# Kernel optimization log

Hardware: AMD Instinct MI355X
Metric: run time of the kernel (lower is better)

## Reference

```python
import jax, jax.numpy as jnp
import numpy as np

B, CIN, COUT = 4, 256, 256
H, W = 48, 48
KH = KW = 7
SH = SW = 1
PH = PW = 3
REL = COUT // 2  # rel_size with groups=1


def setup_inputs() -> dict:
    key = jax.random.key(0)
    ks = jax.random.split(key, 7)
    fan = float(CIN)
    x = jax.random.normal(ks[0], (B, CIN, H, W), jnp.float32)
    w_q = jax.random.normal(ks[1], (COUT, CIN), jnp.float32) * (2.0 / fan) ** 0.5
    w_k = jax.random.normal(ks[2], (COUT, CIN), jnp.float32) * (2.0 / fan) ** 0.5
    w_v = jax.random.normal(ks[3], (COUT, CIN), jnp.float32) * (2.0 / fan) ** 0.5
    bound = 1.0 / np.sqrt(COUT)
    bias = jax.random.uniform(ks[4], (1, COUT, 1, 1), jnp.float32, -bound, bound)
    rel_x = jax.random.normal(ks[5], (REL, KW), jnp.float32)
    rel_y = jax.random.normal(ks[6], (COUT - REL, KH), jnp.float32)
    return {"x": x, "w_q": w_q, "w_k": w_k, "w_v": w_v, "bias": bias,
            "rel_x": rel_x, "rel_y": rel_y}


def reference(x, w_q, w_k, w_v, bias, rel_x, rel_y):
    b = x.shape[0]
    ph, pw = H + 2 * PH, W + 2 * PW
    fh = (ph - KH) // SH + 1
    fw = (pw - KW) // SW + 1
    xp = jnp.pad(x, ((0, 0), (0, 0), (PH, PH), (PW, PW)))
    # 1x1 convs (groups=1) as channel matmuls
    vq = jnp.einsum('oc,bchw->bohw', w_q, xp)
    vk = jnp.einsum('oc,bchw->bohw', w_k, xp)
    vv = jnp.einsum('oc,bchw->bohw', w_v, xp)
    # query at window centers: [b, C, fh, fw]
    win_q = vq[:, :, (KH - 1) // 2: ph - KH // 2: SH, (KW - 1) // 2: pw - KW // 2: SW]
    # relative position terms (sum over channel halves)
    qx = jnp.einsum('bxhw,xk->bhwk', win_q[:, :REL], rel_x)        # [b,fh,fw,kw]
    qy = jnp.einsum('byhw,yk->bhwk', win_q[:, REL:], rel_y)        # [b,fh,fw,kh]
    # overlapping windows via gather (equivalent to torch unfold)
    I = jnp.arange(fh)[:, None] * SH + jnp.arange(KH)[None, :]     # [fh,kh]
    J = jnp.arange(fw)[:, None] * SW + jnp.arange(KW)[None, :]     # [fw,kw]
    win_k = vk[:, :, I[:, None, :, None], J[None, :, None, :]]     # [b,C,fh,fw,kh,kw]
    # channel-summed attention logits (shared across channels, as in source)
    scores = jnp.einsum('bchw,bchwkl->bhwkl', win_q, win_k)
    scores = scores + qy[:, :, :, :, None] + qx[:, :, :, None, :]
    attn = jax.nn.softmax(scores.reshape(b, fh, fw, KH * KW), axis=-1)
    attn = attn.reshape(b, fh, fw, KH, KW)
    win_v = vv[:, :, I[:, None, :, None], J[None, :, None, :]]     # [b,C,fh,fw,kh,kw]
    out = jnp.einsum('bhwkl,bchwkl->bchw', attn, win_v) + bias
    return out
```

## Files before the change

kernel.cpp:

```cpp
#include <hip/hip_runtime.h>

#define BB 4
#define CC 256
#define HH 48
#define WW 48
#define HWHW 2304
#define KK 49
#define RELN 128

#define QSZ (BB*CC*HWHW)
#define ATTNOFF (3*QSZ)
#define SBUF_FLOATS (BB*HH*64*WW)
#define WTOFF (ATTNOFF + SBUF_FLOATS)
#define WT_FLOATS 196608
#define KBOFF (WTOFF + WT_FLOATS)
#define KB_FLOATS 3145728
#define RBOFF (KBOFF + KB_FLOATS)

typedef short bf16x8 __attribute__((ext_vector_type(8)));
typedef float f32x4 __attribute__((ext_vector_type(4)));

__device__ __forceinline__ void split_bf16(float f, unsigned short& hi, unsigned short& lo)
{
    unsigned u = __float_as_uint(f);
    hi = (unsigned short)(u >> 16);
    float r = f - __uint_as_float(u & 0xFFFF0000u);
    unsigned v = __float_as_uint(r);
    v += 0x7FFFu + ((v >> 16) & 1u);
    lo = (unsigned short)(v >> 16);
}

__device__ __forceinline__ void gload16(const uint4* g, uint4* l)
{
    __builtin_amdgcn_global_load_lds(
        (const __attribute__((address_space(1))) void*)g,
        (__attribute__((address_space(3))) void*)l, 16, 0, 0);
}

__global__ __launch_bounds__(256) void prep_kernel(
    const float* __restrict__ x,
    const float* __restrict__ wq, const float* __restrict__ wk,
    const float* __restrict__ wvp,
    const float* __restrict__ relx, const float* __restrict__ rely,
    unsigned short* __restrict__ xt, unsigned short* __restrict__ wt,
    float* __restrict__ ws)
{
    __shared__ unsigned short lds[32*520];
    const int bid = blockIdx.x;
    const int t = threadIdx.x;

    if (bid < 288) {
        const int b = bid / 72;
        const int hw0 = (bid % 72) * 32;
        const int hw = t & 31, cp = t >> 5;
        #pragma unroll 4
        for (int i = 0; i < 32; ++i) {
            int c = i*8 + cp;
            float f = x[((size_t)b*CC + c)*HWHW + hw0 + hw];
            unsigned short hi, lo; split_bf16(f, hi, lo);
            int ch = i*2;
            lds[hw*520 + ((ch       ^ (hw&7))*8) + cp] = hi;
            lds[hw*520 + (((ch + 1) ^ (hw&7))*8) + cp] = lo;
        }
        __syncthreads();
        const int hw2 = t >> 3, u = t & 7;
        uint4* xt4 = (uint4*)xt;
        const size_t rowbase = ((size_t)b*HWHW + hw0 + hw2) * 64;
        #pragma unroll
        for (int j = 0; j < 8; ++j) {
            int chunk = j*8 + u;
            uint4 v = *(const uint4*)&lds[hw2*520 + chunk*8];
            xt4[rowbase + chunk] = v;
        }
        return;
    }
    if (bid < 384) {
        const int tt = (bid - 288)*256 + t;
        const int m = tt >> 5, kg = tt & 31;
        const float* src = (m < 256) ? wq : (m < 512) ? wk : wvp;
        const float* row = src + (size_t)(m & 255)*256 + kg*8;
        unsigned short h[8], l[8];
        #pragma unroll
        for (int j = 0; j < 8; ++j) split_bf16(row[j], h[j], l[j]);
        uint4 hv, lv;
        hv.x = (unsigned)h[0] | ((unsigned)h[1]<<16); hv.y = (unsigned)h[2] | ((unsigned)h[3]<<16);
        hv.z = (unsigned)h[4] | ((unsigned)h[5]<<16); hv.w = (unsigned)h[6] | ((unsigned)h[7]<<16);
        lv.x = (unsigned)l[0] | ((unsigned)l[1]<<16); lv.y = (unsigned)l[2] | ((unsigned)l[3]<<16);
        lv.z = (unsigned)l[4] | ((unsigned)l[5]<<16); lv.w = (unsigned)l[6] | ((unsigned)l[7]<<16);
        uint4* dstrow = (uint4*)wt + (size_t)m*64;
        const int ks = kg >> 2, s_hi = 2*(kg & 3);
        dstrow[ks*8 + ( s_hi      ^ (m&7))] = hv;
        dstrow[ks*8 + ((s_hi + 1) ^ (m&7))] = lv;
        return;
    }
    if (bid < 1152) {
        f32x4* kbz = (f32x4*)(ws + KBOFF);
        int i0 = (bid - 384)*256 + t;
        f32x4 z = (f32x4){0.f,0.f,0.f,0.f};
        #pragma unroll
        for (int it = 0; it < 4; ++it) kbz[i0 + it*196608] = z;
        return;
    }
    {
        unsigned short* rb = (unsigned short*)(ws + RBOFF);
        #pragma unroll
        for (int it = 0; it < 4; ++it) {
            int idx = t + it*256;
            int gi  = idx & 7;
            int l   = (idx >> 3) & 15;
            int ck4 = (idx >> 7) & 3;
            int rel = idx >> 9;
            int isLo = gi >> 2, g4i = gi & 3;
            unsigned short vals[8];
            #pragma unroll
            for (int j = 0; j < 8; ++j) {
                int cl = ck4*32 + g4i*8 + j;
                float f = (l < 7) ? (rel ? rely[cl*7 + l] : relx[cl*7 + l]) : 0.f;
                unsigned short hi, lo; split_bf16(f, hi, lo);
                vals[j] = isLo ? lo : hi;
            }
            int slot = gi ^ (l & 7);
            unsigned short* dst = rb + (((size_t)rel*4 + ck4)*16 + l)*64 + slot*8;
            uint4 pack;
            pack.x = (unsigned)vals[0] | ((unsigned)vals[1]<<16);
            pack.y = (unsigned)vals[2] | ((unsigned)vals[3]<<16);
            pack.z = (unsigned)vals[4] | ((unsigned)vals[5]<<16);
            pack.w = (unsigned)vals[6] | ((unsigned)vals[7]<<16);
            *(uint4*)dst = pack;
        }
    }
}

__global__ __launch_bounds__(256) void proj_gemm_kernel(
    const unsigned short* __restrict__ xt,
    const unsigned short* __restrict__ wt,
    float* __restrict__ ws)
{
    __shared__ uint4 smem[2][1024];
    const int n0 = blockIdx.x * 64;
    const int m0 = blockIdx.y * 64;
    const int b = n0 / HWHW;
    const int hwb = n0 % HWHW;
    const int tid = threadIdx.x;
    const int wid = tid >> 6, ln = tid & 63;
    const int wm = wid >> 1, wn = wid & 1;
    const int l15 = ln & 15, g = ln >> 4;

    f32x4 acc[2][2];
    #pragma unroll
    for (int i = 0; i < 2; ++i)
        #pragma unroll
        for (int j = 0; j < 2; ++j) acc[i][j] = (f32x4){0.f,0.f,0.f,0.f};

    const uint4* wt4 = (const uint4*)wt;
    const uint4* xt4 = (const uint4*)xt;
    const int lrow = ln >> 3, lslot = ln & 7;

    #define STAGE(bf, ks)                                                          \
        {                                                                          \
            _Pragma("unroll")                                                      \
            for (int i = 0; i < 2; ++i) {                                          \
                int seg = wid*2 + i;                                               \
                int row = seg*8 + lrow;                                            \
                gload16(wt4 + (size_t)(m0 + row)*64 + (ks)*8 + lslot,              \
                        &smem[bf][seg*64]);                                        \
                gload16(xt4 + (size_t)(n0 + row)*64 + (ks)*8 + lslot,              \
                        &smem[bf][512 + seg*64]);                                  \
            }                                                                      \
        }

    STAGE(0, 0);
    #pragma unroll
    for (int ks = 0; ks < 8; ++ks) {
        const int cur = ks & 1;
        if (ks < 7) STAGE(cur ^ 1, ks + 1);
        if (ks < 7) asm volatile("s_waitcnt vmcnt(4)" ::: "memory");
        else        asm volatile("s_waitcnt vmcnt(0)" ::: "memory");
        __builtin_amdgcn_s_barrier();
        __builtin_amdgcn_sched_barrier(0);
        bf16x8 aH[2], aL[2], bH[2], bL[2];
        #pragma unroll
        for (int mt = 0; mt < 2; ++mt) {
            int rA = wm*32 + mt*16 + l15;
            aH[mt] = *(const bf16x8*)&smem[cur][rA*8 + ((2*g)   ^ (rA&7))];
            aL[mt] = *(const bf16x8*)&smem[cur][rA*8 + ((2*g+1) ^ (rA&7))];
        }
        #pragma unroll
        for (int nt = 0; nt < 2; ++nt) {
            int rB = wn*32 + nt*16 + l15;
            bH[nt] = *(const bf16x8*)&smem[cur][512 + rB*8 + ((2*g)   ^ (rB&7))];
            bL[nt] = *(const bf16x8*)&smem[cur][512 + rB*8 + ((2*g+1) ^ (rB&7))];
        }
        #pragma unroll
        for (int mt = 0; mt < 2; ++mt)
            #pragma unroll
            for (int nt = 0; nt < 2; ++nt) {
                acc[mt][nt] = __builtin_amdgcn_mfma_f32_16x16x32_bf16(aH[mt], bH[nt], acc[mt][nt], 0, 0, 0);
                acc[mt][nt] = __builtin_amdgcn_mfma_f32_16x16x32_bf16(aH[mt], bL[nt], acc[mt][nt], 0, 0, 0);
                acc[mt][nt] = __builtin_amdgcn_mfma_f32_16x16x32_bf16(aL[mt], bH[nt], acc[mt][nt], 0, 0, 0);
            }
        if (ks < 7) {
            asm volatile("s_waitcnt lgkmcnt(0)" ::: "memory");
            __builtin_amdgcn_s_barrier();
        }
    }
    #undef STAGE

    const int proj = m0 >> 8;
    #pragma unroll
    for (int mt = 0; mt < 2; ++mt) {
        int chb = (m0 & 255) + wm*32 + mt*16 + 4*g;
        #pragma unroll
        for (int nt = 0; nt < 2; ++nt) {
            int hw = hwb + wn*32 + nt*16 + l15;
            f32x4 v = acc[mt][nt];
            if (proj == 2) {
                int ch4 = chb >> 2;
                float* dst = ws + (size_t)2*QSZ + (((size_t)b*64 + ch4)*HWHW + hw)*4;
                *(f32x4*)dst = v;
            } else {
                int hh = hw / 48, w = hw % 48;
                int ck = chb >> 5, p = chb & 31;
                unsigned short h0,h1,h2,h3,l0,l1,l2,l3;
                split_bf16(v[0],h0,l0); split_bf16(v[1],h1,l1);
                split_bf16(v[2],h2,l2); split_bf16(v[3],h3,l3);
                uint2 hv, lv;
                hv.x = (unsigned)h0 | ((unsigned)h1<<16); hv.y = (unsigned)h2 | ((unsigned)h3<<16);
                lv.x = (unsigned)l0 | ((unsigned)l1<<16); lv.y = (unsigned)l2 | ((unsigned)l3<<16);
                int g8 = p >> 3, half = (p >> 2) & 1;
                unsigned short* tb; size_t rowbase; int key;
                if (proj == 0) {
                    tb = (unsigned short*)ws;
                    rowbase = ((((size_t)b*8 + ck)*48 + hh)*48 + w)*64;
                    key = w & 7;
                } else {
                    tb = (unsigned short*)(ws + KBOFF);
                    rowbase = ((((size_t)b*8 + ck)*48 + hh)*64 + (w+3))*64;
                    key = (w+3) & 7;
                }
                *(uint2*)(tb + rowbase + ((g8 ^ key)*8 + half*4))     = hv;
                *(uint2*)(tb + rowbase + (((g8+4) ^ key)*8 + half*4)) = lv;
            }
        }
    }
}

__global__ __launch_bounds__(512) void scores2_kernel(float* __restrict__ ws)
{
    __shared__ unsigned short sAll[4096*8];
    __shared__ float sc[63][48];

    unsigned short* sQ = sAll;
    unsigned short* sK = sAll + 384*8;
    unsigned short* sR = sAll + 3968*8;

    const int bid = blockIdx.x;
    const int b = bid / 48, h = bid % 48;
    const int tid = threadIdx.x;
    const int wv = tid >> 6, ln = tid & 63;
    const int l15 = ln & 15, g4 = ln >> 4;
    const int key = l15 & 7;

    const unsigned short* QB = (const unsigned short*)ws;
    const unsigned short* KB = (const unsigned short*)(ws + KBOFF);
    const unsigned short* RB = (const unsigned short*)(ws + RBOFF);

    for (int u = tid; u < 63*48; u += 512) ((float*)sc)[u] = 0.f;

    const int dk = wv;
    const int hp = h + dk - 3;
    const bool dok = (wv < 7) && (hp >= 0) && (hp < 48);

    f32x4 acc[6], qx[3], qy[3];
    #pragma unroll
    for (int i = 0; i < 6; ++i) acc[i] = (f32x4){0.f,0.f,0.f,0.f};
    #pragma unroll
    for (int i = 0; i < 3; ++i) { qx[i] = (f32x4){0.f,0.f,0.f,0.f}; qy[i] = (f32x4){0.f,0.f,0.f,0.f}; }

    for (int ck = 0; ck < 8; ++ck) {
        #pragma unroll
        for (int e = 0; e < 8; ++e) {
            const int I = wv*8 + e;
            uint4* dst = (uint4*)sAll + I*64;
            if (I < 6) {
                int unit = I*64 + ln; int row = unit >> 3, gr = unit & 7;
                const uint4* src = (const uint4*)QB
                    + ((((size_t)b*8 + ck)*48 + h)*48 + row)*8 + gr;
                gload16(src, dst);
            } else if (I < 62) {
                int uk = (I-6)*64 + ln;
                int kri = uk >> 9;
                int wi = uk & 511; int row = wi >> 3, gr = wi & 7;
                int kh = h + kri - 3;
                if (kh >= 0 && kh < 48) {
                    const uint4* src = (const uint4*)KB
                        + ((((size_t)b*8 + ck)*48 + kh)*64 + row)*8 + gr;
                    gload16(src, dst);
                }
            } else {
                int ur = (I-62)*64 + ln; int row = ur >> 3, gr = ur & 7;
                int rel = ck >> 2, c4 = ck & 3;
                const uint4* src = (const uint4*)RB
                    + (((size_t)rel*4 + c4)*16 + row)*8 + gr;
                gload16(src, dst);
            }
        }
        __syncthreads();

        bf16x8 AH[3], AL[3];
        #pragma unroll
        for (int i = 0; i < 3; ++i) {
            const unsigned short* qr = sQ + (16*i + l15)*64;
            AH[i] = *(const bf16x8*)(qr + ((g4       ^ key)*8));
            AL[i] = *(const bf16x8*)(qr + (((g4 + 4) ^ key)*8));
        }

        if (wv < 7) {
            if (dok) {
                const unsigned short* kbase = sK + dk*4096;
                bf16x8 BH[4], BL[4];
                #pragma unroll
                for (int j = 0; j < 4; ++j) {
                    const unsigned short* kr = kbase + (j*16 + l15)*64;
                    BH[j] = *(const bf16x8*)(kr + ((g4       ^ key)*8));
                    BL[j] = *(const bf16x8*)(kr + (((g4 + 4) ^ key)*8));
                }
                #pragma unroll
                for (int i = 0; i < 3; ++i) {
                    acc[i*2]   = __builtin_amdgcn_mfma_f32_16x16x32_bf16(AH[i], BH[i],   acc[i*2],   0,0,0);
                    acc[i*2]   = __builtin_amdgcn_mfma_f32_16x16x32_bf16(AH[i], BL[i],   acc[i*2],   0,0,0);
                    acc[i*2]   = __builtin_amdgcn_mfma_f32_16x16x32_bf16(AL[i], BH[i],   acc[i*2],   0,0,0);
                    acc[i*2+1] = __builtin_amdgcn_mfma_f32_16x16x32_bf16(AH[i], BH[i+1], acc[i*2+1], 0,0,0);
                    acc[i*2+1] = __builtin_amdgcn_mfma_f32_16x16x32_bf16(AH[i], BL[i+1], acc[i*2+1], 0,0,0);
                    acc[i*2+1] = __builtin_amdgcn_mfma_f32_16x16x32_bf16(AL[i], BH[i+1], acc[i*2+1], 0,0,0);
                }
            }
        } else {
            const unsigned short* rr = sR + l15*64;
            bf16x8 RH = *(const bf16x8*)(rr + ((g4       ^ key)*8));
            bf16x8 RL = *(const bf16x8*)(rr + (((g4 + 4) ^ key)*8));
            if (ck < 4) {
                #pragma unroll
                for (int i = 0; i < 3; ++i) {
                    qx[i] = __builtin_amdgcn_mfma_f32_16x16x32_bf16(AH[i], RH, qx[i], 0,0,0);
                    qx[i] = __builtin_amdgcn_mfma_f32_16x16x32_bf16(AH[i], RL, qx[i], 0,0,0);
                    qx[i] = __builtin_amdgcn_mfma_f32_16x16x32_bf16(AL[i], RH, qx[i], 0,0,0);
                }
            } else {
                #pragma unroll
                for (int i = 0; i < 3; ++i) {
                    qy[i] = __builtin_amdgcn_mfma_f32_16x16x32_bf16(AH[i], RH, qy[i], 0,0,0);
                    qy[i] = __builtin_amdgcn_mfma_f32_16x16x32_bf16(AH[i], RL, qy[i], 0,0,0);
                    qy[i] = __builtin_amdgcn_mfma_f32_16x16x32_bf16(AL[i], RH, qy[i], 0,0,0);
                }
            }
        }
        __syncthreads();
    }

    const int n = l15;
    if (wv < 7) {
        if (dok) {
            #pragma unroll
            for (int i = 0; i < 3; ++i)
                #pragma unroll
                for (int a = 0; a < 2; ++a) {
                    f32x4 A = acc[i*2+a];
                    #pragma unroll
                    for (int r = 0; r < 4; ++r) {
                        int m = 4*g4 + r;
                        int dl = n - m + a*16;
                        if (dl >= 0 && dl < 7)
                            sc[dk*7 + dl][16*i + m] = A[r];
                    }
                }
        }
    } else {
        if (n < 7) {
            #pragma unroll
            for (int i = 0; i < 3; ++i)
                #pragma unroll
                for (int r = 0; r < 4; ++r) {
                    sc[49 + n][16*i + 4*g4 + r] = qx[i][r];
                    sc[56 + n][16*i + 4*g4 + r] = qy[i][r];
                }
        }
    }
    __syncthreads();

    if (tid < 48) {
        const int w = tid;
        float tot[KK], rx[7], ry[7];
        #pragma unroll
        for (int i = 0; i < KK; ++i) tot[i] = sc[i][w];
        #pragma unroll
        for (int l = 0; l < 7; ++l) { rx[l] = sc[49+l][w]; ry[l] = sc[56+l][w]; }
        float mx = -1e30f;
        #pragma unroll
        for (int dk2 = 0; dk2 < 7; ++dk2)
            #pragma unroll
            for (int dl = 0; dl < 7; ++dl) {
                tot[dk2*7+dl] += ry[dk2] + rx[dl];
                mx = fmaxf(mx, tot[dk2*7+dl]);
            }
        float sum = 0.f;
        #pragma unroll
        for (int i = 0; i < KK; ++i) { float e = __expf(tot[i]-mx); tot[i]=e; sum += e; }
        float inv = 1.f/sum;
        float* base = ws + ATTNOFF + ((size_t)(b*HH + h)*64)*WW + w;
        #pragma unroll
        for (int i = 0; i < KK; ++i) base[(size_t)i*WW] = tot[i]*inv;
    }
}

__global__ __launch_bounds__(128) void pv_kernel(
    const float* __restrict__ bias,
    const float* __restrict__ ws,
    float* __restrict__ out)
{
    const float* vbuf = ws + (size_t)2*QSZ;
    const float* attn = ws + ATTNOFF;

    const int bid = blockIdx.x;
    const int pxt = bid % 18;
    const int pgq = (bid / 18) % 16;
    const int b   = bid / (18*16);

    const int tid = threadIdx.x;
    const int pxg = tid & 31;
    const int pg  = pgq*4 + (tid >> 5);

    const int hw0 = pxt*128 + pxg*4;
    const int w0 = hw0 % WW;
    const int h0 = hw0 / WW;

    const float* vb = vbuf + ((size_t)b*64 + pg)*HWHW*4;
    const float* ab = attn + ((size_t)(b*HH + h0)*64)*WW;

    const float4 b4 = *(const float4*)(bias + pg*4);
    f32x4 bias4 = (f32x4){b4.x, b4.y, b4.z, b4.w};
    f32x4 acc[4];
    #pragma unroll
    for (int p = 0; p < 4; ++p) acc[p] = bias4;

    #pragma unroll
    for (int dk = 0; dk < 7; ++dk) {
        const int gr = h0 + dk - 3;
        const bool rok = (gr >= 0 && gr < HH);
        f32x4 vrow[10];
        #pragma unroll
        for (int jj = 0; jj < 10; ++jj) {
            const int gc = w0 - 3 + jj;
            vrow[jj] = (rok && gc >= 0 && gc < WW)
                ? *(const f32x4*)(vb + ((size_t)gr*WW + gc)*4)
                : (f32x4){0.f,0.f,0.f,0.f};
        }
        const float* arow = ab + (size_t)(dk*7)*WW + w0;
        #pragma unroll
        for (int dl = 0; dl < 7; ++dl) {
            const float4 av = *(const float4*)(arow + (size_t)dl*WW);
            acc[0] += vrow[dl+0] * av.x;
            acc[1] += vrow[dl+1] * av.y;
            acc[2] += vrow[dl+2] * av.z;
            acc[3] += vrow[dl+3] * av.w;
        }
    }
    #pragma unroll
    for (int c = 0; c < 4; ++c) {
        float4 o;
        o.x = acc[0][c]; o.y = acc[1][c]; o.z = acc[2][c]; o.w = acc[3][c];
        *(float4*)(out + ((size_t)b*CC + pg*4 + c)*HWHW + hw0) = o;
    }
}

extern "C" void kernel_launch(void* const* d_in, const int* in_sizes, int n_in,
                              void* d_out, int out_size, void* d_ws, size_t ws_size,
                              hipStream_t stream) {
    const float* x    = (const float*)d_in[0];
    const float* wq   = (const float*)d_in[1];
    const float* wk   = (const float*)d_in[2];
    const float* wv   = (const float*)d_in[3];
    const float* bias = (const float*)d_in[4];
    const float* relx = (const float*)d_in[5];
    const float* rely = (const float*)d_in[6];
    float* ws  = (float*)d_ws;
    float* out = (float*)d_out;
    unsigned short* xt = (unsigned short*)d_out;
    unsigned short* wt = (unsigned short*)(ws + WTOFF);

    prep_kernel<<<dim3(1153), dim3(256), 0, stream>>>(x, wq, wk, wv, relx, rely, xt, wt, ws);
    proj_gemm_kernel<<<dim3(144, 12), dim3(256), 0, stream>>>(xt, wt, ws);
    scores2_kernel<<<dim3(BB*HH), dim3(512), 0, stream>>>(ws);
    pv_kernel<<<dim3(BB*16*18), dim3(128), 0, stream>>>(bias, ws, out);
}
```

Before: 75.15 us.

## Stage Q/K epilogue through LDS for coalesced stores; zero only K padding

```diff
diff --git a/kernel.cpp b/kernel.cpp
--- a/kernel.cpp
+++ b/kernel.cpp
@@ -93,12 +93,18 @@
         dstrow[ks*8 + ((s_hi + 1) ^ (m&7))] = lv;
         return;
     }
-    if (bid < 1152) {
-        f32x4* kbz = (f32x4*)(ws + KBOFF);
-        int i0 = (bid - 384)*256 + t;
-        f32x4 z = (f32x4){0.f,0.f,0.f,0.f};
-        #pragma unroll
-        for (int it = 0; it < 4; ++it) kbz[i0 + it*196608] = z;
+    if (bid < 576) {
+        uint4* kb4 = (uint4*)(ws + KBOFF);
+        const uint4 z = make_uint4(0u,0u,0u,0u);
+        int u0 = (bid - 384)*256 + t;
+        #pragma unroll
+        for (int it = 0; it < 4; ++it) {
+            int u = u0 + it*49152;
+            int bch = u >> 7, rem = u & 127;
+            int r16 = rem >> 3, gr = rem & 7;
+            int r = (r16 < 3) ? r16 : 48 + r16;
+            kb4[((size_t)bch*64 + r)*8 + gr] = z;
+        }
         return;
     }
     {
@@ -207,40 +213,67 @@
     #undef STAGE
 
     const int proj = m0 >> 8;
+    if (proj == 2) {
+        #pragma unroll
+        for (int mt = 0; mt < 2; ++mt) {
+            int chb = (m0 & 255) + wm*32 + mt*16 + 4*g;
+            int ch4 = chb >> 2;
+            #pragma unroll
+            for (int nt = 0; nt < 2; ++nt) {
+                int hw = hwb + wn*32 + nt*16 + l15;
+                float* dst = ws + (size_t)2*QSZ + (((size_t)b*64 + ch4)*HWHW + hw)*4;
+                *(f32x4*)dst = acc[mt][nt];
+            }
+        }
+        return;
+    }
+    __syncthreads();
+    unsigned short* eb = (unsigned short*)&smem[0][0];
     #pragma unroll
     for (int mt = 0; mt < 2; ++mt) {
-        int chb = (m0 & 255) + wm*32 + mt*16 + 4*g;
+        const int chb = (m0 & 255) + wm*32 + mt*16 + 4*g;
+        const int ckl = (chb >> 5) & 1;
+        const int p = chb & 31, g8 = p >> 3, half = (p >> 2) & 1;
         #pragma unroll
         for (int nt = 0; nt < 2; ++nt) {
-            int hw = hwb + wn*32 + nt*16 + l15;
+            const int hwl = wn*32 + nt*16 + l15;
+            const int w = (hwb + hwl) % 48;
+            const int key = (proj == 0 ? w : w + 3) & 7;
             f32x4 v = acc[mt][nt];
-            if (proj == 2) {
-                int ch4 = chb >> 2;
-                float* dst = ws + (size_t)2*QSZ + (((size_t)b*64 + ch4)*HWHW + hw)*4;
-                *(f32x4*)dst = v;
-            } else {
-                int hh = hw / 48, w = hw % 48;
-                int ck = chb >> 5, p = chb & 31;
-                unsigned short h0,h1,h2,h3,l0,l1,l2,l3;
-                split_bf16(v[0],h0,l0); split_bf16(v[1],h1,l1);
-                split_bf16(v[2],h2,l2); split_bf16(v[3],h3,l3);
-                uint2 hv, lv;
-                hv.x = (unsigned)h0 | ((unsigned)h1<<16); hv.y = (unsigned)h2 | ((unsigned)h3<<16);
-                lv.x = (unsigned)l0 | ((unsigned)l1<<16); lv.y = (unsigned)l2 | ((unsigned)l3<<16);
-                int g8 = p >> 3, half = (p >> 2) & 1;
-                unsigned short* tb; size_t rowbase; int key;
-                if (proj == 0) {
-                    tb = (unsigned short*)ws;
-                    rowbase = ((((size_t)b*8 + ck)*48 + hh)*48 + w)*64;
-                    key = w & 7;
-                } else {
-                    tb = (unsigned short*)(ws + KBOFF);
-                    rowbase = ((((size_t)b*8 + ck)*48 + hh)*64 + (w+3))*64;
-                    key = (w+3) & 7;
-                }
-                *(uint2*)(tb + rowbase + ((g8 ^ key)*8 + half*4))     = hv;
-                *(uint2*)(tb + rowbase + (((g8+4) ^ key)*8 + half*4)) = lv;
-            }
+            unsigned short h0,h1,h2,h3,q0,q1,q2,q3;
+            split_bf16(v[0],h0,q0); split_bf16(v[1],h1,q1);
+            split_bf16(v[2],h2,q2); split_bf16(v[3],h3,q3);
+            uint2 hv, lv;
+            hv.x = (unsigned)h0 | ((unsigned)h1<<16); hv.y = (unsigned)h2 | ((unsigned)h3<<16);
+            lv.x = (unsigned)q0 | ((unsigned)q1<<16); lv.y = (unsigned)q2 | ((unsigned)q3<<16);
+            const int base = (ckl*64 + hwl)*64;
+            *(uint2*)(eb + base + ((g8 ^ key)*8 + half*4))     = hv;
+            *(uint2*)(eb + base + (((g8+4) ^ key)*8 + half*4)) = lv;
+        }
+    }
+    __syncthreads();
+    const int ck0 = (m0 & 255) >> 5;
+    if (proj == 0) {
+        const uint4* src = (const uint4*)eb;
+        uint4* qb4 = (uint4*)ws;
+        #pragma unroll
+        for (int ckl2 = 0; ckl2 < 2; ++ckl2) {
+            uint4* dst = qb4 + (((size_t)b*8 + ck0 + ckl2)*HWHW + hwb)*8;
+            #pragma unroll
+            for (int it = 0; it < 2; ++it)
+                dst[tid + it*256] = src[ckl2*512 + tid + it*256];
+        }
+    } else {
+        uint4* kb4 = (uint4*)(ws + KBOFF);
+        const uint4* src = (const uint4*)eb;
+        #pragma unroll
+        for (int it = 0; it < 4; ++it) {
+            int u = tid + it*256;
+            int row = u >> 3, gr = u & 7;
+            int ckl2 = row >> 6, hwl2 = row & 63;
+            int hw2 = hwb + hwl2, h2 = hw2/48, w2 = hw2%48;
+            uint4* dst = kb4 + ((((size_t)b*8 + ck0 + ckl2)*48 + h2)*64 + (w2+3))*8;
+            dst[gr] = src[u];
         }
     }
 }
@@ -488,7 +521,7 @@
     unsigned short* xt = (unsigned short*)d_out;
     unsigned short* wt = (unsigned short*)(ws + WTOFF);
 
-    prep_kernel<<<dim3(1153), dim3(256), 0, stream>>>(x, wq, wk, wv, relx, rely, xt, wt, ws);
+    prep_kernel<<<dim3(577), dim3(256), 0, stream>>>(x, wq, wk, wv, relx, rely, xt, wt, ws);
     proj_gemm_kernel<<<dim3(144, 12), dim3(256), 0, stream>>>(xt, wt, ws);
     scores2_kernel<<<dim3(BB*HH), dim3(512), 0, stream>>>(ws);
     pv_kernel<<<dim3(BB*16*18), dim3(128), 0, stream>>>(bias, ws, out);
```

New measurement: 74.91 us. About the same (-0.3%).
